# Kernel tuning notes

Measured on AMD Instinct MI355X. Metric: run time of the kernel, lower is better.

Reference implementation:

```python
import jax, jax.numpy as jnp
import numpy as np

N = 50000      # nodes
E = 800000     # edges
IN_C = 128
HID = 96
OUT_C = 40
L = 8          # num_layers
ALPHA = 0.1
THETA = 0.5
DROPOUT = 0.5


def setup_inputs() -> dict:
    key = jax.random.key(0)
    ks = jax.random.split(key, 6)
    x = jax.random.normal(ks[0], (N, IN_C), dtype=jnp.float32)
    edge_index = jax.random.randint(ks[1], (2, E), 0, N, dtype=jnp.int64)
    proj_w = jax.random.normal(ks[2], (IN_C, HID), dtype=jnp.float32) / np.sqrt(IN_C)
    proj_b = jnp.zeros((HID,), dtype=jnp.float32)
    conv_ws = jax.random.normal(ks[3], (L, HID, HID), dtype=jnp.float32) / np.sqrt(HID)
    out_w = jax.random.normal(ks[4], (2 * HID, OUT_C), dtype=jnp.float32) / np.sqrt(2 * HID)
    out_b = jnp.zeros((OUT_C,), dtype=jnp.float32)
    return {"x": x, "edge_index": edge_index, "proj_w": proj_w, "proj_b": proj_b,
            "conv_ws": conv_ws, "out_w": out_w, "out_b": out_b}


def reference(x, edge_index, proj_w, proj_b, conv_ws, out_w, out_b):
    # --- GCN normalization with self loops (computed once, as GCN2Conv caches it) ---
    loops = jnp.arange(N, dtype=edge_index.dtype)
    src = jnp.concatenate([edge_index[0], loops])   # [E+N]
    dst = jnp.concatenate([edge_index[1], loops])
    deg = jax.ops.segment_sum(jnp.ones(E + N, dtype=x.dtype), dst, num_segments=N)
    dis = jax.lax.rsqrt(deg)                        # deg >= 1 due to self loops
    norm = dis[src] * dis[dst]                      # [E+N]

    h0 = x @ proj_w + proj_b                        # [N, HID]
    h = h0
    key = jax.random.key(42)
    for k in range(L):
        delta = 1.0 / 2 ** k
        kq, ke, kd, key = jax.random.split(key, 4)
        # dithered quantization
        b = (jax.random.uniform(kq, h.shape, dtype=h.dtype) - 0.5) * delta
        h_q = jnp.floor((h + b) / delta) * delta - b
        # GCN2Conv: propagate + initial residual + identity mapping (shared weights)
        agg = jax.ops.segment_sum(h_q[src] * norm[:, None], dst, num_segments=N)
        t = (1.0 - ALPHA) * agg + ALPHA * h0
        beta = float(np.log(THETA / (k + 1) + 1.0))
        h = (1.0 - beta) * t + beta * (t @ conv_ws[k])
        # gaussian noise + relu
        h = jax.nn.relu(h + 0.01 * jax.random.normal(ke, h.shape, dtype=h.dtype))
        if k != L - 1:
            keep = 1.0 - DROPOUT
            mask = jax.random.bernoulli(kd, keep, h.shape)
            h = jnp.where(mask, h / keep, 0.0)
    return jnp.concatenate([h0, h], axis=-1) @ out_w + out_b
```

## Files before the change

### kernel.cpp

```cpp
#include <hip/hip_runtime.h>
#include <hip/hip_fp16.h>
#include <cstdint>
#include <cmath>

#define HID 96
#define INC 128
#define OUTC 40
#define ROWS 32

typedef int      v4i __attribute__((ext_vector_type(4)));
typedef float    v4f __attribute__((ext_vector_type(4)));
typedef unsigned v2u __attribute__((ext_vector_type(2)));

__device__ __forceinline__ int4 ntld_i4(const int* p){
  v4i v = __builtin_nontemporal_load((const v4i*)p);
  return make_int4(v.x, v.y, v.z, v.w);
}
__device__ __forceinline__ float4 ntld_f4(const float* p){
  v4f v = __builtin_nontemporal_load((const v4f*)p);
  return make_float4(v.x, v.y, v.z, v.w);
}
__device__ __forceinline__ void ntst_u2(void* p, unsigned lo, unsigned hi){
  v2u v; v.x = lo; v.y = hi;
  __builtin_nontemporal_store(v, (v2u*)p);
}
__device__ __forceinline__ void ntst_f4(float* p, float a, float b, float c, float d){
  v4f v; v.x = a; v.y = b; v.z = c; v.w = d;
  __builtin_nontemporal_store(v, (v4f*)p);
}

__device__ __forceinline__ unsigned rotl32d(unsigned x, int r){ return (x<<r)|(x>>(32-r)); }

__device__ __forceinline__ void tf2x32_dev(unsigned k0, unsigned k1, unsigned x0, unsigned x1,
                                           unsigned &y0, unsigned &y1){
  unsigned ks2 = k0 ^ k1 ^ 0x1BD11BDAu;
  x0 += k0; x1 += k1;
#define TFR(r) { x0 += x1; x1 = rotl32d(x1, r); x1 ^= x0; }
  TFR(13) TFR(15) TFR(26) TFR(6)   x0 += k1;  x1 += ks2 + 1u;
  TFR(17) TFR(29) TFR(16) TFR(24)  x0 += ks2; x1 += k0 + 2u;
  TFR(13) TFR(15) TFR(26) TFR(6)   x0 += k0;  x1 += k1 + 3u;
  TFR(17) TFR(29) TFR(16) TFR(24)  x0 += k1;  x1 += ks2 + 4u;
  TFR(13) TFR(15) TFR(26) TFR(6)   x0 += ks2; x1 += k0 + 5u;
#undef TFR
  y0 = x0; y1 = x1;
}

__device__ __forceinline__ unsigned tf_bits(unsigned k0, unsigned k1, unsigned idx){
  unsigned y0, y1; tf2x32_dev(k0, k1, 0u, idx, y0, y1); return y0 ^ y1;
}

__device__ __forceinline__ float u01_from_bits(unsigned bits){
  return __uint_as_float((bits >> 9) | 0x3f800000u) - 1.0f;
}

__device__ __forceinline__ float erfinv_xla(float x){
  float w = -log1pf(-x*x);
  float p;
  if (w < 5.0f){
    w = w - 2.5f;
    p = 2.81022636e-08f;
    p = fmaf(p,w, 3.43273939e-07f);
    p = fmaf(p,w,-3.5233877e-06f);
    p = fmaf(p,w,-4.39150654e-06f);
    p = fmaf(p,w, 0.00021858087f);
    p = fmaf(p,w,-0.00125372503f);
    p = fmaf(p,w,-0.00417768164f);
    p = fmaf(p,w, 0.246640727f);
    p = fmaf(p,w, 1.50140941f);
  } else {
    w = sqrtf(w) - 3.0f;
    p = -0.000200214257f;
    p = fmaf(p,w, 0.000100950558f);
    p = fmaf(p,w, 0.00134934322f);
    p = fmaf(p,w,-0.00367342844f);
    p = fmaf(p,w, 0.00573950773f);
    p = fmaf(p,w,-0.0076224613f);
    p = fmaf(p,w, 0.00943887047f);
    p = fmaf(p,w, 1.00167406f);
    p = fmaf(p,w, 2.83297682f);
  }
  return p*x;
}

__global__ void k_detect(const unsigned* __restrict__ raw, int* flag){
  unsigned v = raw[2*threadIdx.x + 1];
  unsigned long long m = __ballot(v == 0u);
  if (threadIdx.x == 0) *flag = (m == 0xFFFFFFFFFFFFFFFFull) ? 1 : 0;
}

__global__ void k_convcount(const unsigned* __restrict__ raw, const int* __restrict__ flag,
                            int E, int* __restrict__ cnt){
  int e = blockIdx.x*256 + threadIdx.x; if (e >= E) return;
  int d;
  if (*flag) d = (int)raw[2*((size_t)E + e)];
  else       d = ((const int*)raw)[E + e];
  atomicAdd(&cnt[d], 1);
}

__global__ void k_hist(const int* __restrict__ cnt, int N, int* __restrict__ bcnt){
  __shared__ int lh[64];
  int tid = threadIdx.x; int n = blockIdx.x*256 + tid;
  if (tid < 64) lh[tid] = 0;
  __syncthreads();
  if (n < N) atomicAdd(&lh[min(cnt[n], 63)], 1);
  __syncthreads();
  if (tid < 64){
    int c = lh[tid];
    if (c > 0) atomicAdd(&bcnt[tid], c);
  }
}

__global__ void k_bucketoff(int* __restrict__ bcnt){
  __shared__ int sb[64];
  int tid = threadIdx.x;
  sb[tid] = bcnt[tid];
  __syncthreads();
  int off = 0;
  for (int b2 = tid+1; b2 < 64; b2++) off += sb[b2];
  bcnt[tid] = off;
}

__global__ void k_perm(const int* __restrict__ cnt, int N, int* __restrict__ boff,
                       int* __restrict__ perm, int* __restrict__ iperm,
                       float* __restrict__ diso, float* __restrict__ dsqr,
                       int* __restrict__ degv, int* __restrict__ degp){
  __shared__ int lh[64];
  int tid = threadIdx.x; int n = blockIdx.x*256 + tid;
  int v = (n < N) ? cnt[n] : 0;
  if (tid < 64) lh[tid] = 0;
  __syncthreads();
  int b = min(v, 63), r = 0;
  if (n < N) r = atomicAdd(&lh[b], 1);
  __syncthreads();
  if (tid < 64){
    int c = lh[tid];
    lh[tid] = (c > 0) ? atomicAdd(&boff[tid], c) : 0;
  }
  __syncthreads();
  if (n < N){
    int pos = lh[b] + r;
    perm[pos] = n;
    iperm[n] = pos;
    diso[n] = 1.0f / sqrtf((float)(v + 1));
    dsqr[pos] = 1.0f / (float)(v + 1);
    degv[pos] = v;
    degp[pos] = (v + 7) & ~7;
  }
}

__global__ void k_scanA(const int* __restrict__ degp, int N, int* __restrict__ psum){
  __shared__ int sh[256];
  int tid = threadIdx.x; int n = blockIdx.x*256 + tid;
  sh[tid] = (n < N) ? degp[n] : 0;
  for (int off = 128; off > 0; off >>= 1){
    __syncthreads();
    if (tid < off) sh[tid] += sh[tid + off];
  }
  __syncthreads();
  if (tid == 0) psum[blockIdx.x] = sh[0];
}

__global__ void k_scanB(int* __restrict__ psum, int nb){
  __shared__ int sh[256];
  int tid = threadIdx.x;
  int v = (tid < nb) ? psum[tid] : 0;
  sh[tid] = v;
  __syncthreads();
  for (int off = 1; off < 256; off <<= 1){
    int t = (tid >= off) ? sh[tid - off] : 0;
    __syncthreads();
    sh[tid] += t;
    __syncthreads();
  }
  if (tid < nb) psum[tid] = sh[tid] - v;
}

__global__ void k_rowptr2(const int* __restrict__ degv, const int* __restrict__ degp,
                          const int* __restrict__ psum, int N,
                          int* __restrict__ rowptr, int* __restrict__ csr_src,
                          float* __restrict__ csr_w){
  __shared__ int sh[256];
  int tid = threadIdx.x; int n = blockIdx.x*256 + tid;
  int vp = (n < N) ? degp[n] : 0;
  sh[tid] = vp;
  __syncthreads();
  for (int off = 1; off < 256; off <<= 1){
    int t = (tid >= off) ? sh[tid - off] : 0;
    __syncthreads();
    sh[tid] += t;
    __syncthreads();
  }
  if (n < N){
    int base = psum[blockIdx.x] + sh[tid] - vp;
    rowptr[n] = base;
    int v = degv[n];
    for (int q = v; q < vp; q++){ csr_src[base + q] = 0; csr_w[base + q] = 0.0f; }
    if (n == N-1) rowptr[N] = base + vp;
  }
}

__global__ void k_fill(const unsigned* __restrict__ raw, const int* __restrict__ flag, int E,
                       const int* __restrict__ rowptr, const int* __restrict__ iperm,
                       int* __restrict__ cur, const float* __restrict__ diso,
                       int* __restrict__ csr_src, float* __restrict__ csr_w){
  int e = blockIdx.x*256 + threadIdx.x; if (e >= E) return;
  int s, d;
  if (*flag){ s = (int)raw[2*(size_t)e]; d = (int)raw[2*((size_t)E + e)]; }
  else      { const int* r = (const int*)raw; s = r[e]; d = r[E + e]; }
  int rd = iperm[d];
  int pos = atomicAdd(&cur[rd], 1);
  int slot = rowptr[rd] + pos;
  csr_src[slot] = iperm[s];
  csr_w[slot] = diso[s]*diso[d];
}

__global__ __launch_bounds__(256) void k_h0(
  const float* __restrict__ x, const float* __restrict__ W, const float* __restrict__ bias,
  const int* __restrict__ iperm,
  float* __restrict__ h0p, __half* __restrict__ hq, unsigned kq0, unsigned kq1, int N)
{
  __shared__ float xs[64*65];
  __shared__ float wsh[64*96];
  int tid = threadIdx.x; int n0 = blockIdx.x*64;
  int cg = tid & 15, ng = tid >> 4; int c0 = cg*6;
  float acc[4][6];
#pragma unroll
  for (int i=0;i<4;i++) for (int j=0;j<6;j++) acc[i][j]=0.f;
  for (int kc=0; kc<2; kc++){
    if (kc) __syncthreads();
    for (int q=tid; q<1536; q+=256)
      ((float4*)wsh)[q] = ((const float4*)(W + kc*64*96))[q];
    for (int q=tid; q<1024; q+=256){
      int g=q*4; int r=g>>6, col=g&63;
      int n=n0+r; int ns = n<N ? n : N-1;
      float4 v = ((const float4*)(x + (size_t)ns*128 + kc*64))[col>>2];
      xs[r*65+col]=v.x; xs[r*65+col+1]=v.y; xs[r*65+col+2]=v.z; xs[r*65+col+3]=v.w;
    }
    __syncthreads();
    for (int k=0;k<64;k++){
      float wv[6];
#pragma unroll
      for (int j=0;j<6;j++) wv[j]=wsh[k*96 + c0 + j];
#pragma unroll
      for (int i=0;i<4;i++){
        float xv = xs[(ng*4+i)*65 + k];
#pragma unroll
        for (int j=0;j<6;j++) acc[i][j] = fmaf(xv, wv[j], acc[i][j]);
      }
    }
  }
#pragma unroll
  for (int i=0;i<4;i++){
    int n = n0 + ng*4 + i; if (n >= N) continue;
    int rn = iperm[n];
#pragma unroll
    for (int j=0;j<6;j++){
      int c = c0 + j; int p = n*96 + c;
      float v = acc[i][j] + bias[c];
      h0p[(size_t)rn*96 + c] = v;
      unsigned bq = tf_bits(kq0, kq1, (unsigned)p);
      float b = u01_from_bits(bq) - 0.5f;
      hq[(size_t)rn*96 + c] = __float2half_rn(floorf(v + b) - b);
    }
  }
}

#define GATH(gj, wv) { \
  float2 f01 = __half22float2(*(__half2*)&gj.x); \
  float2 f23 = __half22float2(*(__half2*)&gj.y); \
  ax = fmaf(f01.x, wv, ax); ay = fmaf(f01.y, wv, ay); \
  az = fmaf(f23.x, wv, az); aw = fmaf(f23.y, wv, aw); }

__global__ __launch_bounds__(256, 7) void k_layer(
  const __half* __restrict__ hq_in, const float* __restrict__ h0p, const float* __restrict__ dsqr,
  const int* __restrict__ rowptr, const int* __restrict__ csr_src, const float* __restrict__ csr_w,
  const int* __restrict__ perm, const float* __restrict__ W,
  float betaf, float ombf,
  unsigned ke0, unsigned ke1, unsigned kd0, unsigned kd1,
  unsigned kq0, unsigned kq1, float delta_n, float invdelta_n,
  int do_dropout, int write_h,
  __half* __restrict__ hq_out, float* __restrict__ h_out, int N)
{
  __shared__ float ts[ROWS*100];
  __shared__ float wsh[24*96];
  int tid = threadIdx.x;
  int tx = tid & 31, ty = tid >> 5;
  int n0 = blockIdx.x*ROWS;

  const char* hqc = (const char*)hq_in;

#pragma unroll 1
  for (int pass = 0; pass < 4; pass++){
    int r = pass*8 + ty;
    int row = n0 + r;
    if (tx < 24){
      float4 o = make_float4(0.f, 0.f, 0.f, 0.f);
      if (row < N){
        unsigned txb = (unsigned)tx*8u;
        float dd = dsqr[row];
        unsigned lo = (unsigned)rowptr[row], hi = (unsigned)rowptr[row+1];
        uint2 sraw = *(const uint2*)(hqc + (unsigned)row*192u + txb);
        float4 hz = ntld_f4(h0p + (size_t)row*96 + tx*4);
        float2 s01 = __half22float2(*(__half2*)&sraw.x);
        float2 s23 = __half22float2(*(__half2*)&sraw.y);
        float ax = s01.x*dd, ay = s01.y*dd, az = s23.x*dd, aw = s23.y*dd;
        unsigned s = lo;
        unsigned n16 = lo + ((hi - lo) & ~15u);
        for (; s < n16; s += 16){
          int4   sa = ntld_i4(csr_src + s);
          int4   sb = ntld_i4(csr_src + s + 4);
          int4   sc = ntld_i4(csr_src + s + 8);
          int4   sd = ntld_i4(csr_src + s + 12);
          float4 wa = ntld_f4(csr_w + s);
          float4 wb = ntld_f4(csr_w + s + 4);
          float4 wc = ntld_f4(csr_w + s + 8);
          float4 wd = ntld_f4(csr_w + s + 12);
          uint2 g0 = *(const uint2*)(hqc + (unsigned)sa.x*192u + txb);
          uint2 g1 = *(const uint2*)(hqc + (unsigned)sa.y*192u + txb);
          uint2 g2 = *(const uint2*)(hqc + (unsigned)sa.z*192u + txb);
          uint2 g3 = *(const uint2*)(hqc + (unsigned)sa.w*192u + txb);
          uint2 g4 = *(const uint2*)(hqc + (unsigned)sb.x*192u + txb);
          uint2 g5 = *(const uint2*)(hqc + (unsigned)sb.y*192u + txb);
          uint2 g6 = *(const uint2*)(hqc + (unsigned)sb.z*192u + txb);
          uint2 g7 = *(const uint2*)(hqc + (unsigned)sb.w*192u + txb);
          uint2 g8 = *(const uint2*)(hqc + (unsigned)sc.x*192u + txb);
          uint2 g9 = *(const uint2*)(hqc + (unsigned)sc.y*192u + txb);
          uint2 gA = *(const uint2*)(hqc + (unsigned)sc.z*192u + txb);
          uint2 gB = *(const uint2*)(hqc + (unsigned)sc.w*192u + txb);
          uint2 gC = *(const uint2*)(hqc + (unsigned)sd.x*192u + txb);
          uint2 gD = *(const uint2*)(hqc + (unsigned)sd.y*192u + txb);
          uint2 gE = *(const uint2*)(hqc + (unsigned)sd.z*192u + txb);
          uint2 gF = *(const uint2*)(hqc + (unsigned)sd.w*192u + txb);
          GATH(g0, wa.x) GATH(g1, wa.y) GATH(g2, wa.z) GATH(g3, wa.w)
          GATH(g4, wb.x) GATH(g5, wb.y) GATH(g6, wb.z) GATH(g7, wb.w)
          GATH(g8, wc.x) GATH(g9, wc.y) GATH(gA, wc.z) GATH(gB, wc.w)
          GATH(gC, wd.x) GATH(gD, wd.y) GATH(gE, wd.z) GATH(gF, wd.w)
        }
        for (; s < hi; s += 8){
          int4   sa = ntld_i4(csr_src + s);
          int4   sb = ntld_i4(csr_src + s + 4);
          float4 wa = ntld_f4(csr_w + s);
          float4 wb = ntld_f4(csr_w + s + 4);
          uint2 g0 = *(const uint2*)(hqc + (unsigned)sa.x*192u + txb);
          uint2 g1 = *(const uint2*)(hqc + (unsigned)sa.y*192u + txb);
          uint2 g2 = *(const uint2*)(hqc + (unsigned)sa.z*192u + txb);
          uint2 g3 = *(const uint2*)(hqc + (unsigned)sa.w*192u + txb);
          uint2 g4 = *(const uint2*)(hqc + (unsigned)sb.x*192u + txb);
          uint2 g5 = *(const uint2*)(hqc + (unsigned)sb.y*192u + txb);
          uint2 g6 = *(const uint2*)(hqc + (unsigned)sb.z*192u + txb);
          uint2 g7 = *(const uint2*)(hqc + (unsigned)sb.w*192u + txb);
          GATH(g0, wa.x) GATH(g1, wa.y) GATH(g2, wa.z) GATH(g3, wa.w)
          GATH(g4, wb.x) GATH(g5, wb.y) GATH(g6, wb.z) GATH(g7, wb.w)
        }
        o.x = 0.9f*ax + 0.1f*hz.x;
        o.y = 0.9f*ay + 0.1f*hz.y;
        o.z = 0.9f*az + 0.1f*hz.z;
        o.w = 0.9f*aw + 0.1f*hz.w;
      }
      *((float4*)&ts[r*100 + tx*4]) = o;
    }
  }

  int cg = tid & 7, ng = tid >> 3;
  int c0 = cg * 12;
  float acc[12];
#pragma unroll
  for (int j = 0; j < 12; j++) acc[j] = 0.f;

  for (int chunk = 0; chunk < 4; chunk++){
    __syncthreads();
    for (int q = tid; q < 576; q += 256)
      ((float4*)wsh)[q] = ((const float4*)(W + chunk*24*96))[q];
    __syncthreads();
#pragma unroll 4
    for (int kk = 0; kk < 24; kk++){
      int k = chunk*24 + kk;
      float4 w0 = *((const float4*)&wsh[kk*96 + c0]);
      float4 w1 = *((const float4*)&wsh[kk*96 + c0 + 4]);
      float4 w2 = *((const float4*)&wsh[kk*96 + c0 + 8]);
      float xv = ts[ng*100 + k];
      acc[0] = fmaf(xv, w0.x, acc[0]);  acc[1] = fmaf(xv, w0.y, acc[1]);
      acc[2] = fmaf(xv, w0.z, acc[2]);  acc[3] = fmaf(xv, w0.w, acc[3]);
      acc[4] = fmaf(xv, w1.x, acc[4]);  acc[5] = fmaf(xv, w1.y, acc[5]);
      acc[6] = fmaf(xv, w1.z, acc[6]);  acc[7] = fmaf(xv, w1.w, acc[7]);
      acc[8] = fmaf(xv, w2.x, acc[8]);  acc[9] = fmaf(xv, w2.y, acc[9]);
      acc[10]= fmaf(xv, w2.z, acc[10]); acc[11]= fmaf(xv, w2.w, acc[11]);
    }
  }

  const float LO = __uint_as_float(0xBF7FFFFFu);
  int n = n0 + ng;
  if (n < N){
    int po = perm[n];
    float res[12];
#pragma unroll
    for (int j = 0; j < 12; j++){
      int c = c0 + j; unsigned p = (unsigned)po*96u + (unsigned)c;
      float tv = ts[ng*100 + c];
      float hv = ombf*tv + betaf*acc[j];
      unsigned be = tf_bits(ke0, ke1, p);
      float uv = fmaxf(LO, u01_from_bits(be)*2.0f + LO);
      hv += 0.01f * (1.41421356f * erfinv_xla(uv));
      hv = fmaxf(hv, 0.0f);
      if (do_dropout){
        unsigned bd = tf_bits(kd0, kd1, p);
        hv = (bd < 0x80000000u) ? hv*2.0f : 0.0f;
      }
      if (!write_h){
        unsigned bq = tf_bits(kq0, kq1, p);
        float b = (u01_from_bits(bq) - 0.5f)*delta_n;
        hv = floorf((hv + b)*invdelta_n)*delta_n - b;
      }
      res[j] = hv;
    }
    if (write_h){
      float* dst2 = h_out + (size_t)n*96 + c0;
#pragma unroll
      for (int j4 = 0; j4 < 3; j4++)
        ntst_f4(&dst2[j4*4], res[j4*4], res[j4*4+1], res[j4*4+2], res[j4*4+3]);
    } else {
      __half* dst2 = hq_out + (size_t)n*96 + c0;
#pragma unroll
      for (int j4 = 0; j4 < 3; j4++){
        unsigned lo2 = (unsigned)__half_as_ushort(__float2half_rn(res[j4*4+0]))
                     | ((unsigned)__half_as_ushort(__float2half_rn(res[j4*4+1])) << 16);
        unsigned hi2 = (unsigned)__half_as_ushort(__float2half_rn(res[j4*4+2]))
                     | ((unsigned)__half_as_ushort(__float2half_rn(res[j4*4+3])) << 16);
        ntst_u2(dst2 + j4*4, lo2, hi2);
      }
    }
  }
}

__global__ __launch_bounds__(256) void k_final(
  const float* __restrict__ h0p, const float* __restrict__ hp,
  const float* __restrict__ W, const float* __restrict__ bias,
  const int* __restrict__ perm, float* __restrict__ out, int N)
{
  __shared__ float xs[64*97];
  __shared__ float wsh[96*40];
  int tid = threadIdx.x; int n0 = blockIdx.x*64;
  int cg = tid & 7, ng = tid >> 3; int c0 = cg*5;
  float acc[2][5];
#pragma unroll
  for (int i=0;i<2;i++) for (int j=0;j<5;j++) acc[i][j]=0.f;
  for (int ph=0; ph<2; ph++){
    if (ph) __syncthreads();
    const float* xsrc = ph ? hp : h0p;
    for (int q=tid; q<960; q+=256)
      ((float4*)wsh)[q] = ((const float4*)(W + ph*96*40))[q];
    for (int q=tid; q<1536; q+=256){
      int g=q*4; int r=g/96, col=g%96;
      int n=n0+r; int ns = n<N ? n : N-1;
      float4 v = ((const float4*)(xsrc + (size_t)ns*96))[col>>2];
      xs[r*97+col]=v.x; xs[r*97+col+1]=v.y; xs[r*97+col+2]=v.z; xs[r*97+col+3]=v.w;
    }
    __syncthreads();
    for (int k=0;k<96;k++){
      float wv[5];
#pragma unroll
      for (int j=0;j<5;j++) wv[j]=wsh[k*40 + c0 + j];
#pragma unroll
      for (int i=0;i<2;i++){
        float xv = xs[(ng*2+i)*97 + k];
#pragma unroll
        for (int j=0;j<5;j++) acc[i][j] = fmaf(xv, wv[j], acc[i][j]);
      }
    }
  }
#pragma unroll
  for (int i=0;i<2;i++){
    int n = n0 + ng*2 + i; if (n >= N) continue;
    int pm = perm[n];
#pragma unroll
    for (int j=0;j<5;j++)
      out[(size_t)pm*40 + c0 + j] = acc[i][j] + bias[c0 + j];
  }
}

static void tf_host(uint32_t k0, uint32_t k1, uint32_t x0, uint32_t x1,
                    uint32_t &y0, uint32_t &y1){
  uint32_t ks2 = k0 ^ k1 ^ 0x1BD11BDAu;
  x0 += k0; x1 += k1;
  auto R = [&](int r){ x0 += x1; x1 = (x1<<r)|(x1>>(32-r)); x1 ^= x0; };
  R(13);R(15);R(26);R(6);   x0 += k1;  x1 += ks2 + 1u;
  R(17);R(29);R(16);R(24);  x0 += ks2; x1 += k0 + 2u;
  R(13);R(15);R(26);R(6);   x0 += k0;  x1 += k1 + 3u;
  R(17);R(29);R(16);R(24);  x0 += k1;  x1 += ks2 + 4u;
  R(13);R(15);R(26);R(6);   x0 += ks2; x1 += k0 + 5u;
  y0 = x0; y1 = x1;
}

extern "C" void kernel_launch(void* const* d_in, const int* in_sizes, int n_in,
                              void* d_out, int out_size, void* d_ws, size_t ws_size,
                              hipStream_t stream)
{
  const float*    x       = (const float*)d_in[0];
  const unsigned* eraw    = (const unsigned*)d_in[1];
  const float*    proj_w  = (const float*)d_in[2];
  const float*    proj_b  = (const float*)d_in[3];
  const float*    conv_w  = (const float*)d_in[4];
  const float*    out_w   = (const float*)d_in[5];
  const float*    out_b   = (const float*)d_in[6];
  float* out = (float*)d_out;

  const int N = in_sizes[0] / INC;
  const int E = in_sizes[1] / 2;
  const size_t NH = (size_t)N * HID;
  const int NP = (N + 16) & ~15;
  const int EP = ((E + 7*N + 15) & ~15);

  float*  ws     = (float*)d_ws;
  float*  h0p    = ws;
  float*  hbp    = h0p + NH;
  __half* hqA    = (__half*)(hbp + NH);
  __half* hqB    = hqA + NH;
  float*  csr_w  = (float*)(hqB + NH);
  int*    csr_src= (int*)(csr_w + EP);
  int*    rowptr = csr_src + EP;
  int*    perm   = rowptr + NP;
  int*    iperm  = perm + NP;
  int*    degv   = iperm + NP;
  int*    degp   = degv + NP;
  int*    cnt    = degp + NP;
  int*    cur    = cnt + NP;
  float*  diso   = (float*)(cur + NP);
  float*  dsqr   = diso + NP;
  int*    bcnt   = (int*)(dsqr + NP);
  int*    psum   = bcnt + 64;
  int*    flag   = psum + 256;
  (void)ws_size; (void)n_in; (void)out_size;

  uint32_t kq[8][2], ke[8][2], kd[8][2];
  {
    uint32_t K0 = 0u, K1 = 42u;
    for (int k = 0; k < 8; k++){
      uint32_t y0, y1;
      tf_host(K0, K1, 0u, 0u, y0, y1); kq[k][0]=y0; kq[k][1]=y1;
      tf_host(K0, K1, 0u, 1u, y0, y1); ke[k][0]=y0; ke[k][1]=y1;
      tf_host(K0, K1, 0u, 2u, y0, y1); kd[k][0]=y0; kd[k][1]=y1;
      tf_host(K0, K1, 0u, 3u, y0, y1); K0=y0; K1=y1;
    }
  }

  const int gE  = (E + 255)/256;
  const int gN  = (N + 255)/256;
  const int gMM = (N + 63)/64;
  const int gL  = (N + ROWS-1)/ROWS;

  hipMemsetAsync(cnt, 0, (size_t)N*4, stream);
  hipMemsetAsync(bcnt, 0, 64*4, stream);
  k_detect   <<<1, 64, 0, stream>>>(eraw, flag);
  k_convcount<<<gE, 256, 0, stream>>>(eraw, flag, E, cnt);
  k_hist     <<<gN, 256, 0, stream>>>(cnt, N, bcnt);
  k_bucketoff<<<1, 64, 0, stream>>>(bcnt);
  k_perm     <<<gN, 256, 0, stream>>>(cnt, N, bcnt, perm, iperm, diso, dsqr, degv, degp);
  k_scanA    <<<gN, 256, 0, stream>>>(degp, N, psum);
  k_scanB    <<<1, 256, 0, stream>>>(psum, gN);
  k_rowptr2  <<<gN, 256, 0, stream>>>(degv, degp, psum, N, rowptr, csr_src, csr_w);
  hipMemsetAsync(cur, 0, (size_t)N*4, stream);
  k_fill     <<<gE, 256, 0, stream>>>(eraw, flag, E, rowptr, iperm, cur, diso, csr_src, csr_w);

  k_h0<<<gMM, 256, 0, stream>>>(x, proj_w, proj_b, iperm, h0p, hqA, kq[0][0], kq[0][1], N);

  for (int k = 0; k < 8; k++){
    double bd = log(0.5/(double)(k+1) + 1.0);
    float betaf = (float)bd;
    float ombf  = (float)(1.0 - bd);
    int last = (k == 7);
    float dn  = 1.0f/(float)(1 << (k+1));
    float idn = (float)(1 << (k+1));
    const __half* hin  = (k & 1) ? hqB : hqA;
    __half*       hout = (k & 1) ? hqA : hqB;
    k_layer<<<gL, 256, 0, stream>>>(hin, h0p, dsqr, rowptr, csr_src, csr_w, perm,
      conv_w + (size_t)k*HID*HID, betaf, ombf,
      ke[k][0], ke[k][1], kd[k][0], kd[k][1],
      last?0u:kq[k+1][0], last?0u:kq[k+1][1], dn, idn,
      !last, last, hout, hbp, N);
  }

  k_final<<<gMM, 256, 0, stream>>>(h0p, hbp, out_w, out_b, perm, out, N);
}
```

Baseline: 988.3 us.

## Split fused layer kernel into separate gather and dense-transform kernels

```diff
diff --git a/kernel.cpp b/kernel.cpp
--- a/kernel.cpp
+++ b/kernel.cpp
@@ -271,9 +271,77 @@
   ax = fmaf(f01.x, wv, ax); ay = fmaf(f01.y, wv, ay); \
   az = fmaf(f23.x, wv, az); aw = fmaf(f23.y, wv, aw); }
 
-__global__ __launch_bounds__(256, 7) void k_layer(
-  const __half* __restrict__ hq_in, const float* __restrict__ h0p, const float* __restrict__ dsqr,
-  const int* __restrict__ rowptr, const int* __restrict__ csr_src, const float* __restrict__ csr_w,
+__global__ __launch_bounds__(256, 8) void k_gather(
+  const __half* __restrict__ hq_in, const float* __restrict__ dsqr,
+  const int* __restrict__ rowptr, const int* __restrict__ csr_src,
+  const float* __restrict__ csr_w, float* __restrict__ tbuf, int N)
+{
+  int tid = threadIdx.x;
+  int tx = tid & 31, ty = tid >> 5;
+  int row = blockIdx.x*8 + ty;
+  if (row >= N || tx >= 24) return;
+
+  const char* hqc = (const char*)hq_in;
+  unsigned txb = (unsigned)tx*8u;
+  float dd = dsqr[row];
+  unsigned lo = (unsigned)rowptr[row], hi = (unsigned)rowptr[row+1];
+  uint2 sraw = *(const uint2*)(hqc + (unsigned)row*192u + txb);
+  float2 s01 = __half22float2(*(__half2*)&sraw.x);
+  float2 s23 = __half22float2(*(__half2*)&sraw.y);
+  float ax = s01.x*dd, ay = s01.y*dd, az = s23.x*dd, aw = s23.y*dd;
+  unsigned s = lo;
+  unsigned n16 = lo + ((hi - lo) & ~15u);
+  for (; s < n16; s += 16){
+    int4   sa = ntld_i4(csr_src + s);
+    int4   sb = ntld_i4(csr_src + s + 4);
+    int4   sc = ntld_i4(csr_src + s + 8);
+    int4   sd = ntld_i4(csr_src + s + 12);
+    float4 wa = ntld_f4(csr_w + s);
+    float4 wb = ntld_f4(csr_w + s + 4);
+    float4 wc = ntld_f4(csr_w + s + 8);
+    float4 wd = ntld_f4(csr_w + s + 12);
+    uint2 g0 = *(const uint2*)(hqc + (unsigned)sa.x*192u + txb);
+    uint2 g1 = *(const uint2*)(hqc + (unsigned)sa.y*192u + txb);
+    uint2 g2 = *(const uint2*)(hqc + (unsigned)sa.z*192u + txb);
+    uint2 g3 = *(const uint2*)(hqc + (unsigned)sa.w*192u + txb);
+    uint2 g4 = *(const uint2*)(hqc + (unsigned)sb.x*192u + txb);
+    uint2 g5 = *(const uint2*)(hqc + (unsigned)sb.y*192u + txb);
+    uint2 g6 = *(const uint2*)(hqc + (unsigned)sb.z*192u + txb);
+    uint2 g7 = *(const uint2*)(hqc + (unsigned)sb.w*192u + txb);
+    uint2 g8 = *(const uint2*)(hqc + (unsigned)sc.x*192u + txb);
+    uint2 g9 = *(const uint2*)(hqc + (unsigned)sc.y*192u + txb);
+    uint2 gA = *(const uint2*)(hqc + (unsigned)sc.z*192u + txb);
+    uint2 gB = *(const uint2*)(hqc + (unsigned)sc.w*192u + txb);
+    uint2 gC = *(const uint2*)(hqc + (unsigned)sd.x*192u + txb);
+    uint2 gD = *(const uint2*)(hqc + (unsigned)sd.y*192u + txb);
+    uint2 gE = *(const uint2*)(hqc + (unsigned)sd.z*192u + txb);
+    uint2 gF = *(const uint2*)(hqc + (unsigned)sd.w*192u + txb);
+    GATH(g0, wa.x) GATH(g1, wa.y) GATH(g2, wa.z) GATH(g3, wa.w)
+    GATH(g4, wb.x) GATH(g5, wb.y) GATH(g6, wb.z) GATH(g7, wb.w)
+    GATH(g8, wc.x) GATH(g9, wc.y) GATH(gA, wc.z) GATH(gB, wc.w)
+    GATH(gC, wd.x) GATH(gD, wd.y) GATH(gE, wd.z) GATH(gF, wd.w)
+  }
+  for (; s < hi; s += 8){
+    int4   sa = ntld_i4(csr_src + s);
+    int4   sb = ntld_i4(csr_src + s + 4);
+    float4 wa = ntld_f4(csr_w + s);
+    float4 wb = ntld_f4(csr_w + s + 4);
+    uint2 g0 = *(const uint2*)(hqc + (unsigned)sa.x*192u + txb);
+    uint2 g1 = *(const uint2*)(hqc + (unsigned)sa.y*192u + txb);
+    uint2 g2 = *(const uint2*)(hqc + (unsigned)sa.z*192u + txb);
+    uint2 g3 = *(const uint2*)(hqc + (unsigned)sa.w*192u + txb);
+    uint2 g4 = *(const uint2*)(hqc + (unsigned)sb.x*192u + txb);
+    uint2 g5 = *(const uint2*)(hqc + (unsigned)sb.y*192u + txb);
+    uint2 g6 = *(const uint2*)(hqc + (unsigned)sb.z*192u + txb);
+    uint2 g7 = *(const uint2*)(hqc + (unsigned)sb.w*192u + txb);
+    GATH(g0, wa.x) GATH(g1, wa.y) GATH(g2, wa.z) GATH(g3, wa.w)
+    GATH(g4, wb.x) GATH(g5, wb.y) GATH(g6, wb.z) GATH(g7, wb.w)
+  }
+  ntst_f4(tbuf + (size_t)row*96 + tx*4, ax, ay, az, aw);
+}
+
+__global__ __launch_bounds__(256, 7) void k_mm(
+  const float* __restrict__ tbuf, const float* __restrict__ h0p,
   const int* __restrict__ perm, const float* __restrict__ W,
   float betaf, float ombf,
   unsigned ke0, unsigned ke1, unsigned kd0, unsigned kd1,
@@ -284,81 +352,17 @@
   __shared__ float ts[ROWS*100];
   __shared__ float wsh[24*96];
   int tid = threadIdx.x;
-  int tx = tid & 31, ty = tid >> 5;
   int n0 = blockIdx.x*ROWS;
 
-  const char* hqc = (const char*)hq_in;
-
-#pragma unroll 1
-  for (int pass = 0; pass < 4; pass++){
-    int r = pass*8 + ty;
-    int row = n0 + r;
-    if (tx < 24){
-      float4 o = make_float4(0.f, 0.f, 0.f, 0.f);
-      if (row < N){
-        unsigned txb = (unsigned)tx*8u;
-        float dd = dsqr[row];
-        unsigned lo = (unsigned)rowptr[row], hi = (unsigned)rowptr[row+1];
-        uint2 sraw = *(const uint2*)(hqc + (unsigned)row*192u + txb);
-        float4 hz = ntld_f4(h0p + (size_t)row*96 + tx*4);
-        float2 s01 = __half22float2(*(__half2*)&sraw.x);
-        float2 s23 = __half22float2(*(__half2*)&sraw.y);
-        float ax = s01.x*dd, ay = s01.y*dd, az = s23.x*dd, aw = s23.y*dd;
-        unsigned s = lo;
-        unsigned n16 = lo + ((hi - lo) & ~15u);
-        for (; s < n16; s += 16){
-          int4   sa = ntld_i4(csr_src + s);
-          int4   sb = ntld_i4(csr_src + s + 4);
-          int4   sc = ntld_i4(csr_src + s + 8);
-          int4   sd = ntld_i4(csr_src + s + 12);
-          float4 wa = ntld_f4(csr_w + s);
-          float4 wb = ntld_f4(csr_w + s + 4);
-          float4 wc = ntld_f4(csr_w + s + 8);
-          float4 wd = ntld_f4(csr_w + s + 12);
-          uint2 g0 = *(const uint2*)(hqc + (unsigned)sa.x*192u + txb);
-          uint2 g1 = *(const uint2*)(hqc + (unsigned)sa.y*192u + txb);
-          uint2 g2 = *(const uint2*)(hqc + (unsigned)sa.z*192u + txb);
-          uint2 g3 = *(const uint2*)(hqc + (unsigned)sa.w*192u + txb);
-          uint2 g4 = *(const uint2*)(hqc + (unsigned)sb.x*192u + txb);
-          uint2 g5 = *(const uint2*)(hqc + (unsigned)sb.y*192u + txb);
-          uint2 g6 = *(const uint2*)(hqc + (unsigned)sb.z*192u + txb);
-          uint2 g7 = *(const uint2*)(hqc + (unsigned)sb.w*192u + txb);
-          uint2 g8 = *(const uint2*)(hqc + (unsigned)sc.x*192u + txb);
-          uint2 g9 = *(const uint2*)(hqc + (unsigned)sc.y*192u + txb);
-          uint2 gA = *(const uint2*)(hqc + (unsigned)sc.z*192u + txb);
-          uint2 gB = *(const uint2*)(hqc + (unsigned)sc.w*192u + txb);
-          uint2 gC = *(const uint2*)(hqc + (unsigned)sd.x*192u + txb);
-          uint2 gD = *(const uint2*)(hqc + (unsigned)sd.y*192u + txb);
-          uint2 gE = *(const uint2*)(hqc + (unsigned)sd.z*192u + txb);
-          uint2 gF = *(const uint2*)(hqc + (unsigned)sd.w*192u + txb);
-          GATH(g0, wa.x) GATH(g1, wa.y) GATH(g2, wa.z) GATH(g3, wa.w)
-          GATH(g4, wb.x) GATH(g5, wb.y) GATH(g6, wb.z) GATH(g7, wb.w)
-          GATH(g8, wc.x) GATH(g9, wc.y) GATH(gA, wc.z) GATH(gB, wc.w)
-          GATH(gC, wd.x) GATH(gD, wd.y) GATH(gE, wd.z) GATH(gF, wd.w)
-        }
-        for (; s < hi; s += 8){
-          int4   sa = ntld_i4(csr_src + s);
-          int4   sb = ntld_i4(csr_src + s + 4);
-          float4 wa = ntld_f4(csr_w + s);
-          float4 wb = ntld_f4(csr_w + s + 4);
-          uint2 g0 = *(const uint2*)(hqc + (unsigned)sa.x*192u + txb);
-          uint2 g1 = *(const uint2*)(hqc + (unsigned)sa.y*192u + txb);
-          uint2 g2 = *(const uint2*)(hqc + (unsigned)sa.z*192u + txb);
-          uint2 g3 = *(const uint2*)(hqc + (unsigned)sa.w*192u + txb);
-          uint2 g4 = *(const uint2*)(hqc + (unsigned)sb.x*192u + txb);
-          uint2 g5 = *(const uint2*)(hqc + (unsigned)sb.y*192u + txb);
-          uint2 g6 = *(const uint2*)(hqc + (unsigned)sb.z*192u + txb);
-          uint2 g7 = *(const uint2*)(hqc + (unsigned)sb.w*192u + txb);
-          GATH(g0, wa.x) GATH(g1, wa.y) GATH(g2, wa.z) GATH(g3, wa.w)
-          GATH(g4, wb.x) GATH(g5, wb.y) GATH(g6, wb.z) GATH(g7, wb.w)
-        }
-        o.x = 0.9f*ax + 0.1f*hz.x;
-        o.y = 0.9f*ay + 0.1f*hz.y;
-        o.z = 0.9f*az + 0.1f*hz.z;
-        o.w = 0.9f*aw + 0.1f*hz.w;
-      }
-      *((float4*)&ts[r*100 + tx*4]) = o;
-    }
+  for (int q = tid; q < 768; q += 256){
+    int g = q*4; int r = g/96, col = g%96;
+    int n = n0 + r; int ns = n < N ? n : N-1;
+    float4 a = *(const float4*)(tbuf + (size_t)ns*96 + col);
+    float4 z = *(const float4*)(h0p  + (size_t)ns*96 + col);
+    ts[r*100+col+0] = 0.9f*a.x + 0.1f*z.x;
+    ts[r*100+col+1] = 0.9f*a.y + 0.1f*z.y;
+    ts[r*100+col+2] = 0.9f*a.z + 0.1f*z.z;
+    ts[r*100+col+3] = 0.9f*a.w + 0.1f*z.w;
   }
 
   int cg = tid & 7, ng = tid >> 3;
@@ -529,6 +533,7 @@
   int*    bcnt   = (int*)(dsqr + NP);
   int*    psum   = bcnt + 64;
   int*    flag   = psum + 256;
+  float*  tbuf   = hbp;
   (void)ws_size; (void)n_in; (void)out_size;
 
   uint32_t kq[8][2], ke[8][2], kd[8][2];
@@ -546,6 +551,7 @@
   const int gE  = (E + 255)/256;
   const int gN  = (N + 255)/256;
   const int gMM = (N + 63)/64;
+  const int gG  = (N + 7)/8;
   const int gL  = (N + ROWS-1)/ROWS;
 
   hipMemsetAsync(cnt, 0, (size_t)N*4, stream);
@@ -572,7 +578,8 @@
     float idn = (float)(1 << (k+1));
     const __half* hin  = (k & 1) ? hqB : hqA;
     __half*       hout = (k & 1) ? hqA : hqB;
-    k_layer<<<gL, 256, 0, stream>>>(hin, h0p, dsqr, rowptr, csr_src, csr_w, perm,
+    k_gather<<<gG, 256, 0, stream>>>(hin, dsqr, rowptr, csr_src, csr_w, tbuf, N);
+    k_mm    <<<gL, 256, 0, stream>>>(tbuf, h0p, perm,
       conv_w + (size_t)k*HID*HID, betaf, ombf,
       ke[k][0], ke[k][1], kd[k][0], kd[k][1],
       last?0u:kq[k+1][0], last?0u:kq[k+1][1], dn, idn,
```

Result: slower. 1.185 ms (+19.9%).
